# Performance work log

Measured on AMD Instinct MI355X. Metric: run time of the kernel, lower is better.

The kernel has to match this reference:

```python
import jax, jax.numpy as jnp
import numpy as np

B, T, F, H, O = 64, 2048, 128, 512, 4
G = 4 * H  # gates: i, f, g, o (PyTorch order)


def setup_inputs() -> dict:
    key = jax.random.key(0)
    ks = jax.random.split(key, 12)
    s = 1.0 / np.sqrt(H)  # PyTorch LSTM init scale
    return {
        "x": jax.random.normal(ks[0], (B, T, F), dtype=jnp.float32),
        "W_ih_l0": jax.random.uniform(ks[1], (G, F), jnp.float32, -s, s),
        "W_hh_l0": jax.random.uniform(ks[2], (G, H), jnp.float32, -s, s),
        "b_ih_l0": jax.random.uniform(ks[3], (G,), jnp.float32, -s, s),
        "b_hh_l0": jax.random.uniform(ks[4], (G,), jnp.float32, -s, s),
        "W_ih_l1": jax.random.uniform(ks[5], (G, H), jnp.float32, -s, s),
        "W_hh_l1": jax.random.uniform(ks[6], (G, H), jnp.float32, -s, s),
        "b_ih_l1": jax.random.uniform(ks[7], (G,), jnp.float32, -s, s),
        "b_hh_l1": jax.random.uniform(ks[8], (G,), jnp.float32, -s, s),
        "W_out": jax.random.uniform(ks[9], (O, H), jnp.float32, -s, s),
        "b_out": jax.random.uniform(ks[10], (O,), jnp.float32, -s, s),
    }


def lstm_layer(x_seq, W_ih, W_hh, b_ih, b_hh):
    # x_seq: [B, T, Fin] -> (h_seq [B, T, H], h_final [B, H])
    b = x_seq.shape[0]
    h_dim = W_hh.shape[1]
    # Precompute input projections for all timesteps in one big GEMM.
    x_proj = jnp.einsum('btf,gf->btg', x_seq, W_ih) + b_ih + b_hh  # [B, T, 4H]

    def step(carry, xp_t):
        h, c = carry
        gates = xp_t + h @ W_hh.T  # [B, 4H]
        i, f, g, o = jnp.split(gates, 4, axis=-1)
        i = jax.nn.sigmoid(i)
        f = jax.nn.sigmoid(f)
        g = jnp.tanh(g)
        o = jax.nn.sigmoid(o)
        c = f * c + i * g
        h = o * jnp.tanh(c)
        return (h, c), h

    h0 = jnp.zeros((b, h_dim), x_seq.dtype)
    c0 = jnp.zeros((b, h_dim), x_seq.dtype)
    (hT, _), hs = jax.lax.scan(step, (h0, c0), jnp.swapaxes(x_proj, 0, 1))
    return jnp.swapaxes(hs, 0, 1), hT


def reference(x, W_ih_l0, W_hh_l0, b_ih_l0, b_hh_l0,
              W_ih_l1, W_hh_l1, b_ih_l1, b_hh_l1, W_out, b_out):
    h0_seq, h0_final = lstm_layer(x, W_ih_l0, W_hh_l0, b_ih_l0, b_hh_l0)
    _, h1_final = lstm_layer(h0_seq, W_ih_l1, W_hh_l1, b_ih_l1, b_hh_l1)
    # hn = stack([h0_final, h1_final]); relu(hn); linear applied to hn[0]
    hn0 = jax.nn.relu(h0_final)  # [B, H]
    out = hn0 @ W_out.T + b_out  # [B, 4]
    return out
```

## Files before the change

### kernel.cpp

```cpp
#include <hip/hip_runtime.h>
#include <hip/hip_bf16.h>
#include <cstdint>
#include <cstddef>


#define B_ 64
#define T_ 2048
#define F_ 128
#define H_ 512

#define NBLK 128
#define NTHR 256

#define ACT_STRIDE 1280
#define SMEM_SZ (16 * ACT_STRIDE)
#define HSLOT (B_ * H_)

typedef __bf16 bf16;
typedef __bf16 bf16x4 __attribute__((ext_vector_type(4)));
typedef __bf16 bf16x8 __attribute__((ext_vector_type(8)));
typedef float f32x4 __attribute__((ext_vector_type(4)));
typedef unsigned int u32;
typedef u32 u32x2 __attribute__((ext_vector_type(2)));
typedef u32 u32x4 __attribute__((ext_vector_type(4)));

static __device__ __forceinline__ float sigm(float v) {
  return 1.f / (1.f + __expf(-v));
}
static __device__ __forceinline__ float tanh_f(float v) {
  float a = fminf(fabsf(v), 20.f);
  float e = __expf(-2.f * a);
  float t = 1.f - 2.f * e / (1.f + e);
  return copysignf(t, v);
}
static __device__ __forceinline__ u32 bf16bits(float f) {
  bf16 b = (bf16)f;
  unsigned short us;
  __builtin_memcpy(&us, &b, 2);
  return (u32)us;
}

__global__ void __launch_bounds__(NTHR) prep_kernel(u32* hbuf) {
  int idx = blockIdx.x * blockDim.x + threadIdx.x;
  hbuf[idx] = 0u;
}

__global__ void __launch_bounds__(NTHR) xconv_kernel(
    const float* __restrict__ x, bf16* __restrict__ xbf) {
  const int b = blockIdx.x;
  const int t0 = blockIdx.y * 256;
  const int f2 = threadIdx.x & 63;
  const int tq = threadIdx.x >> 6;
  const int rg = b >> 4, row = b & 15;
  for (int i = 0; i < 64; ++i) {
    int t = t0 + i * 4 + tq;
    float2 xv = *(const float2*)(x + ((size_t)b * T_ + t) * F_ + 2 * f2);
    u32 w = bf16bits(xv.x) | (bf16bits(xv.y) << 16);
    *(u32*)((char*)xbf + ((((size_t)t * 4 + rg) * 16 + row) * 128 + 2 * f2) * 2) = w;
  }
}

__global__ void __launch_bounds__(NTHR, 1) lstm_kernel(
    const float* __restrict__ x,
    const float* __restrict__ Wih,
    const float* __restrict__ Whh,
    const float* __restrict__ bih,
    const float* __restrict__ bhh,
    u32* __restrict__ hbuf,
    float* __restrict__ hf32,
    const bf16* __restrict__ xbf)
{
  __shared__ __align__(16) char smem[SMEM_SZ];

  const int tid = threadIdx.x;
  const int bid = blockIdx.x;
  const int rg = bid >> 5;
  const int jg = bid & 31;
  const int row0 = rg * 16;
  const int j0 = jg * 16;

  const int lane = tid & 63;
  const int wave = tid >> 6;
  const int fr = lane & 15;
  const int kg = lane >> 4;

  bf16x8 wfrag[20];
  {
    const int G = (fr >> 2) * H_ + j0 + wave * 4 + (fr & 3);
    const float* sih = Wih + (size_t)G * F_;
    const float* shh = Whh + (size_t)G * H_;
    #pragma unroll
    for (int kk = 0; kk < 20; ++kk) {
      const float* s = (kk < 4) ? (sih + kk * 32 + kg * 8)
                                : (shh + (kk - 4) * 32 + kg * 8);
      float4 f0 = *(const float4*)s;
      float4 f1 = *(const float4*)(s + 4);
      bf16x8 w = { (bf16)f0.x, (bf16)f0.y, (bf16)f0.z, (bf16)f0.w,
                   (bf16)f1.x, (bf16)f1.y, (bf16)f1.z, (bf16)f1.w };
      wfrag[kk] = w;
    }
  }

  const int jcol = j0 + wave * 4 + kg;
  const float bi_ = bih[0 * H_ + jcol] + bhh[0 * H_ + jcol];
  const float bf_ = bih[1 * H_ + jcol] + bhh[1 * H_ + jcol];
  const float bg_ = bih[2 * H_ + jcol] + bhh[2 * H_ + jcol];
  const float bo_ = bih[3 * H_ + jcol] + bhh[3 * H_ + jcol];

  const int prow = tid >> 4;
  const int pw = tid & 15;
  const int r0x = tid >> 5;
  const int c40 = tid & 31;
  const float* xp0 = x + (size_t)(row0 + r0x) * T_ * F_ + c40 * 4;
  const float* xp1 = x + (size_t)(row0 + r0x + 8) * T_ * F_ + c40 * 4;
  const int xw0 = r0x * ACT_STRIDE + ((8 * c40) ^ ((r0x & 7) << 4));
  const int xw1 = (r0x + 8) * ACT_STRIDE + ((8 * c40) ^ (((r0x + 8) & 7) << 4));
  const int xrow = tid >> 4;
  const int xseg = tid & 15;
  const int xw = xrow * ACT_STRIDE + ((xseg * 16) ^ ((xrow & 7) << 4));

  char* buf = smem;
  float c_state = 0.f;

  for (int t = 0; t < T_; ++t) {
    if (xbf) {
      u32x4 xv = *(const u32x4*)((const char*)xbf
                  + ((size_t)t * 4 + rg) * 4096 + tid * 16);
      *(u32x4*)(buf + xw) = xv;
    } else {
      float4 xv0 = *(const float4*)(xp0 + (size_t)t * F_);
      float4 xv1 = *(const float4*)(xp1 + (size_t)t * F_);
      bf16x4 b0 = { (bf16)xv0.x, (bf16)xv0.y, (bf16)xv0.z, (bf16)xv0.w };
      bf16x4 b1 = { (bf16)xv1.x, (bf16)xv1.y, (bf16)xv1.z, (bf16)xv1.w };
      *(bf16x4*)(buf + xw0) = b0;
      *(bf16x4*)(buf + xw1) = b1;
    }
    __syncthreads();

    u32x4 v0, v1, v2, v3, v4, v5, v6, v7;
    const u32* hb = hbuf + (size_t)(t & 1) * HSLOT + (size_t)(row0 + prow) * H_ + 4 * pw;
    #define ISSUE_POLLS()                                                               \
      asm volatile("global_load_dwordx4 %0, %1, off sc0 sc1" : "=v"(v0) : "v"(hb));      \
      asm volatile("global_load_dwordx4 %0, %1, off offset:256 sc0 sc1" : "=v"(v1) : "v"(hb)); \
      asm volatile("global_load_dwordx4 %0, %1, off offset:512 sc0 sc1" : "=v"(v2) : "v"(hb)); \
      asm volatile("global_load_dwordx4 %0, %1, off offset:768 sc0 sc1" : "=v"(v3) : "v"(hb)); \
      asm volatile("global_load_dwordx4 %0, %1, off offset:1024 sc0 sc1" : "=v"(v4) : "v"(hb)); \
      asm volatile("global_load_dwordx4 %0, %1, off offset:1280 sc0 sc1" : "=v"(v5) : "v"(hb)); \
      asm volatile("global_load_dwordx4 %0, %1, off offset:1536 sc0 sc1" : "=v"(v6) : "v"(hb)); \
      asm volatile("global_load_dwordx4 %0, %1, off offset:1792 sc0 sc1" : "=v"(v7) : "v"(hb))
    ISSUE_POLLS();
    __builtin_amdgcn_sched_barrier(0);

    f32x4 a0 = {0.f, 0.f, 0.f, 0.f}, a1 = {0.f, 0.f, 0.f, 0.f};
    const char* bbase = buf + fr * ACT_STRIDE;
    const int bmask = (fr & 7) << 4;
    {
      bf16x8 p0 = *(const bf16x8*)(bbase + ((0 * 64 + kg * 16) ^ bmask));
      a0 = __builtin_amdgcn_mfma_f32_16x16x32_bf16(wfrag[0], p0, a0, 0, 0, 0);
      bf16x8 p1 = *(const bf16x8*)(bbase + ((1 * 64 + kg * 16) ^ bmask));
      a1 = __builtin_amdgcn_mfma_f32_16x16x32_bf16(wfrag[1], p1, a1, 0, 0, 0);
      bf16x8 p2 = *(const bf16x8*)(bbase + ((2 * 64 + kg * 16) ^ bmask));
      a0 = __builtin_amdgcn_mfma_f32_16x16x32_bf16(wfrag[2], p2, a0, 0, 0, 0);
      bf16x8 p3 = *(const bf16x8*)(bbase + ((3 * 64 + kg * 16) ^ bmask));
      a1 = __builtin_amdgcn_mfma_f32_16x16x32_bf16(wfrag[3], p3, a1, 0, 0, 0);
    }
    __builtin_amdgcn_sched_barrier(0);

    {
      const u32 tgt = (u32)t << 16;
      for (;;) {
        asm volatile("s_waitcnt vmcnt(0)" ::: "memory");
        __builtin_amdgcn_sched_barrier(0);
        u32 m0 = v0[0]; m0 = m0 < v0[1] ? m0 : v0[1];
        u32 m1 = v0[2]; m1 = m1 < v0[3] ? m1 : v0[3];
        #define MIN4(V) { m0 = m0 < V[0] ? m0 : V[0]; m0 = m0 < V[1] ? m0 : V[1]; \
                          m1 = m1 < V[2] ? m1 : V[2]; m1 = m1 < V[3] ? m1 : V[3]; }
        MIN4(v1) MIN4(v2) MIN4(v3) MIN4(v4) MIN4(v5) MIN4(v6) MIN4(v7)
        #undef MIN4
        u32 m = m0 < m1 ? m0 : m1;
        if (m >= tgt) break;
        ISSUE_POLLS();
      }
    }
    #undef ISSUE_POLLS

    {
      char* dst = buf + prow * ACT_STRIDE;
      const int swz = (prow & 7) << 4;
      #define UNPACK(i, V)                                                  \
        {                                                                   \
          u32 w0 = (V[0] & 0xffffu) | (V[1] << 16);                         \
          u32 w1 = (V[2] & 0xffffu) | (V[3] << 16);                         \
          u32x2 wp = { w0, w1 };                                            \
          *(u32x2*)(dst + ((256 + 128 * (i) + 8 * pw) ^ swz)) = wp;         \
        }
      UNPACK(0, v0) UNPACK(1, v1) UNPACK(2, v2) UNPACK(3, v3)
      UNPACK(4, v4) UNPACK(5, v5) UNPACK(6, v6) UNPACK(7, v7)
      #undef UNPACK
    }
    __syncthreads();

    #pragma unroll
    for (int kk = 4; kk < 20; kk += 2) {
      bf16x8 b0 = *(const bf16x8*)(bbase + ((kk * 64 + kg * 16) ^ bmask));
      a0 = __builtin_amdgcn_mfma_f32_16x16x32_bf16(wfrag[kk], b0, a0, 0, 0, 0);
      bf16x8 b1 = *(const bf16x8*)(bbase + (((kk + 1) * 64 + kg * 16) ^ bmask));
      a1 = __builtin_amdgcn_mfma_f32_16x16x32_bf16(wfrag[kk + 1], b1, a1, 0, 0, 0);
    }
    f32x4 dsum = a0 + a1;

    float d0 = dsum[0], d1 = dsum[1], d2 = dsum[2], d3 = dsum[3];
    float t0 = __shfl_xor((kg & 2) ? d0 : d2, 32, 64);
    float t1 = __shfl_xor((kg & 2) ? d1 : d3, 32, 64);
    float w0 = (kg & 2) ? t0 : d0;
    float w1 = (kg & 2) ? t1 : d1;
    float w2 = (kg & 2) ? d2 : t0;
    float w3 = (kg & 2) ? d3 : t1;
    float t2 = __shfl_xor((kg & 1) ? w0 : w1, 16, 64);
    float t3 = __shfl_xor((kg & 1) ? w2 : w3, 16, 64);
    float gi = (kg & 1) ? t2 : w0;
    float gf = (kg & 1) ? w1 : t2;
    float gg = (kg & 1) ? t3 : w2;
    float go = (kg & 1) ? w3 : t3;

    float iv = sigm(gi + bi_);
    float fv = sigm(gf + bf_);
    float gv = tanh_f(gg + bg_);
    float ov = sigm(go + bo_);
    c_state = fv * c_state + iv * gv;
    float hv = ov * tanh_f(c_state);

    u32 val = ((u32)(t + 1) << 16) | bf16bits(hv);
    u32* dstp = hbuf + (size_t)((t + 1) & 1) * HSLOT + (size_t)(row0 + fr) * H_ + jcol;
    asm volatile("global_store_dword %0, %1, off sc0 sc1" :: "v"(dstp), "v"(val) : "memory");

    if (t == T_ - 1) hf32[(size_t)(row0 + fr) * H_ + jcol] = hv;
  }
}

__global__ void __launch_bounds__(64) out_kernel(
    const float* __restrict__ h_f32,
    const float* __restrict__ Wout,
    const float* __restrict__ bout,
    float* __restrict__ out)
{
  int b = blockIdx.x;
  int lane = threadIdx.x;
  float a0 = 0.f, a1 = 0.f, a2 = 0.f, a3 = 0.f;
  for (int j = lane; j < H_; j += 64) {
    float hv = fmaxf(h_f32[(size_t)b * H_ + j], 0.f);
    a0 += hv * Wout[0 * H_ + j];
    a1 += hv * Wout[1 * H_ + j];
    a2 += hv * Wout[2 * H_ + j];
    a3 += hv * Wout[3 * H_ + j];
  }
  #pragma unroll
  for (int off = 32; off; off >>= 1) {
    a0 += __shfl_down(a0, off);
    a1 += __shfl_down(a1, off);
    a2 += __shfl_down(a2, off);
    a3 += __shfl_down(a3, off);
  }
  if (lane == 0) {
    out[b * 4 + 0] = a0 + bout[0];
    out[b * 4 + 1] = a1 + bout[1];
    out[b * 4 + 2] = a2 + bout[2];
    out[b * 4 + 3] = a3 + bout[3];
  }
}

extern "C" void kernel_launch(void* const* d_in, const int* in_sizes, int n_in,
                              void* d_out, int out_size, void* d_ws, size_t ws_size,
                              hipStream_t stream) {
  const float* x    = (const float*)d_in[0];
  const float* Wih  = (const float*)d_in[1];
  const float* Whh  = (const float*)d_in[2];
  const float* bih  = (const float*)d_in[3];
  const float* bhh  = (const float*)d_in[4];
  const float* Wout = (const float*)d_in[9];
  const float* bout = (const float*)d_in[10];

  char* ws = (char*)d_ws;
  u32*   hbuf = (u32*)ws;
  float* hf32 = (float*)(ws + 262144);
  const size_t XBF_OFF = 393216;
  const size_t XBF_SZ = (size_t)T_ * 4 * 16 * 128 * 2;
  bf16* xbf = (ws_size >= XBF_OFF + XBF_SZ) ? (bf16*)(ws + XBF_OFF) : nullptr;

  hipLaunchKernelGGL(prep_kernel, dim3(256), dim3(NTHR), 0, stream, hbuf);
  if (xbf)
    hipLaunchKernelGGL(xconv_kernel, dim3(64, 8), dim3(NTHR), 0, stream, x, xbf);

  void* args[] = { (void*)&x, (void*)&Wih, (void*)&Whh, (void*)&bih, (void*)&bhh,
                   (void*)&hbuf, (void*)&hf32, (void*)&xbf };
  hipLaunchCooperativeKernel((void*)lstm_kernel, dim3(NBLK), dim3(NTHR),
                             args, 0, stream);

  hipLaunchKernelGGL(out_kernel, dim3(B_), dim3(64), 0, stream,
                     hf32, Wout, bout, (float*)d_out);
}
```

Measured before the change: 4.204 ms.

## Replace tagged-hidden-state polling with per-step arrival counters and packed bf16 h

The old scheme embedded a step tag in each 32-bit h word, so every wave polled and min-reduced 8 dwordx4 loads per iteration. Now h is stored as plain bf16 and each wave increments a per-row-group counter after its store. Consumers spin on a single counter dword, then fetch half as many h bytes and write them straight to LDS without unpacking. This adds an extra waitcnt plus an atomic per wave per step, serialises the h fetch behind the counter, and includes a guard break that could silently proceed on timeout.

Result: slower. 7.285 ms (+73.3%).

```diff
diff --git a/kernel.cpp b/kernel.cpp
--- a/kernel.cpp
+++ b/kernel.cpp
@@ -14,14 +14,12 @@
 
 #define ACT_STRIDE 1280
 #define SMEM_SZ (16 * ACT_STRIDE)
-#define HSLOT (B_ * H_)
 
 typedef __bf16 bf16;
 typedef __bf16 bf16x4 __attribute__((ext_vector_type(4)));
 typedef __bf16 bf16x8 __attribute__((ext_vector_type(8)));
 typedef float f32x4 __attribute__((ext_vector_type(4)));
 typedef unsigned int u32;
-typedef u32 u32x2 __attribute__((ext_vector_type(2)));
 typedef u32 u32x4 __attribute__((ext_vector_type(4)));
 
 static __device__ __forceinline__ float sigm(float v) {
@@ -40,9 +38,10 @@
   return (u32)us;
 }
 
-__global__ void __launch_bounds__(NTHR) prep_kernel(u32* hbuf) {
+__global__ void __launch_bounds__(NTHR) prep_kernel(u32* hbuf_words, u32* cnt) {
   int idx = blockIdx.x * blockDim.x + threadIdx.x;
-  hbuf[idx] = 0u;
+  hbuf_words[idx] = 0u;
+  if (idx < 16384) cnt[idx] = ((idx & 4095) == 0) ? 128u : 0u;
 }
 
 __global__ void __launch_bounds__(NTHR) xconv_kernel(
@@ -66,7 +65,8 @@
     const float* __restrict__ Whh,
     const float* __restrict__ bih,
     const float* __restrict__ bhh,
-    u32* __restrict__ hbuf,
+    bf16* __restrict__ hbuf,
+    u32* __restrict__ cnt,
     float* __restrict__ hf32,
     const bf16* __restrict__ xbf)
 {
@@ -115,99 +115,90 @@
   const float* xp1 = x + (size_t)(row0 + r0x + 8) * T_ * F_ + c40 * 4;
   const int xw0 = r0x * ACT_STRIDE + ((8 * c40) ^ ((r0x & 7) << 4));
   const int xw1 = (r0x + 8) * ACT_STRIDE + ((8 * c40) ^ (((r0x + 8) & 7) << 4));
-  const int xrow = tid >> 4;
-  const int xseg = tid & 15;
-  const int xw = xrow * ACT_STRIDE + ((xseg * 16) ^ ((xrow & 7) << 4));
-
-  char* buf = smem;
+  const int xw = prow * ACT_STRIDE + ((pw * 16) ^ ((prow & 7) << 4));
+
+  const char* bbase = smem + fr * ACT_STRIDE;
+  const int bmask = (fr & 7) << 4;
+  u32* cgrp = cnt + (rg << 12);
+
   float c_state = 0.f;
 
   for (int t = 0; t < T_; ++t) {
     if (xbf) {
       u32x4 xv = *(const u32x4*)((const char*)xbf
                   + ((size_t)t * 4 + rg) * 4096 + tid * 16);
-      *(u32x4*)(buf + xw) = xv;
+      *(u32x4*)(smem + xw) = xv;
     } else {
       float4 xv0 = *(const float4*)(xp0 + (size_t)t * F_);
       float4 xv1 = *(const float4*)(xp1 + (size_t)t * F_);
       bf16x4 b0 = { (bf16)xv0.x, (bf16)xv0.y, (bf16)xv0.z, (bf16)xv0.w };
       bf16x4 b1 = { (bf16)xv1.x, (bf16)xv1.y, (bf16)xv1.z, (bf16)xv1.w };
-      *(bf16x4*)(buf + xw0) = b0;
-      *(bf16x4*)(buf + xw1) = b1;
+      *(bf16x4*)(smem + xw0) = b0;
+      *(bf16x4*)(smem + xw1) = b1;
     }
     __syncthreads();
 
-    u32x4 v0, v1, v2, v3, v4, v5, v6, v7;
-    const u32* hb = hbuf + (size_t)(t & 1) * HSLOT + (size_t)(row0 + prow) * H_ + 4 * pw;
-    #define ISSUE_POLLS()                                                               \
-      asm volatile("global_load_dwordx4 %0, %1, off sc0 sc1" : "=v"(v0) : "v"(hb));      \
-      asm volatile("global_load_dwordx4 %0, %1, off offset:256 sc0 sc1" : "=v"(v1) : "v"(hb)); \
-      asm volatile("global_load_dwordx4 %0, %1, off offset:512 sc0 sc1" : "=v"(v2) : "v"(hb)); \
-      asm volatile("global_load_dwordx4 %0, %1, off offset:768 sc0 sc1" : "=v"(v3) : "v"(hb)); \
-      asm volatile("global_load_dwordx4 %0, %1, off offset:1024 sc0 sc1" : "=v"(v4) : "v"(hb)); \
-      asm volatile("global_load_dwordx4 %0, %1, off offset:1280 sc0 sc1" : "=v"(v5) : "v"(hb)); \
-      asm volatile("global_load_dwordx4 %0, %1, off offset:1536 sc0 sc1" : "=v"(v6) : "v"(hb)); \
-      asm volatile("global_load_dwordx4 %0, %1, off offset:1792 sc0 sc1" : "=v"(v7) : "v"(hb))
-    ISSUE_POLLS();
-    __builtin_amdgcn_sched_barrier(0);
+    u32 cv;
+    const u32* cp = cgrp + t;
+    asm volatile("global_load_dword %0, %1, off sc0 sc1" : "=v"(cv) : "v"(cp));
 
     f32x4 a0 = {0.f, 0.f, 0.f, 0.f}, a1 = {0.f, 0.f, 0.f, 0.f};
-    const char* bbase = buf + fr * ACT_STRIDE;
-    const int bmask = (fr & 7) << 4;
+    f32x4 a2 = {0.f, 0.f, 0.f, 0.f}, a3 = {0.f, 0.f, 0.f, 0.f};
     {
       bf16x8 p0 = *(const bf16x8*)(bbase + ((0 * 64 + kg * 16) ^ bmask));
       a0 = __builtin_amdgcn_mfma_f32_16x16x32_bf16(wfrag[0], p0, a0, 0, 0, 0);
       bf16x8 p1 = *(const bf16x8*)(bbase + ((1 * 64 + kg * 16) ^ bmask));
       a1 = __builtin_amdgcn_mfma_f32_16x16x32_bf16(wfrag[1], p1, a1, 0, 0, 0);
-      bf16x8 p2 = *(const bf16x8*)(bbase + ((2 * 64 + kg * 16) ^ bmask));
-      a0 = __builtin_amdgcn_mfma_f32_16x16x32_bf16(wfrag[2], p2, a0, 0, 0, 0);
-      bf16x8 p3 = *(const bf16x8*)(bbase + ((3 * 64 + kg * 16) ^ bmask));
-      a1 = __builtin_amdgcn_mfma_f32_16x16x32_bf16(wfrag[3], p3, a1, 0, 0, 0);
-    }
-    __builtin_amdgcn_sched_barrier(0);
-
-    {
-      const u32 tgt = (u32)t << 16;
+    }
+    {
+      int guard = 0;
       for (;;) {
         asm volatile("s_waitcnt vmcnt(0)" ::: "memory");
         __builtin_amdgcn_sched_barrier(0);
-        u32 m0 = v0[0]; m0 = m0 < v0[1] ? m0 : v0[1];
-        u32 m1 = v0[2]; m1 = m1 < v0[3] ? m1 : v0[3];
-        #define MIN4(V) { m0 = m0 < V[0] ? m0 : V[0]; m0 = m0 < V[1] ? m0 : V[1]; \
-                          m1 = m1 < V[2] ? m1 : V[2]; m1 = m1 < V[3] ? m1 : V[3]; }
-        MIN4(v1) MIN4(v2) MIN4(v3) MIN4(v4) MIN4(v5) MIN4(v6) MIN4(v7)
-        #undef MIN4
-        u32 m = m0 < m1 ? m0 : m1;
-        if (m >= tgt) break;
-        ISSUE_POLLS();
+        if (cv >= 128u) break;
+        if (++guard > (1 << 22)) break;
+        asm volatile("global_load_dword %0, %1, off sc0 sc1" : "=v"(cv) : "v"(cp));
       }
     }
-    #undef ISSUE_POLLS
-
-    {
-      char* dst = buf + prow * ACT_STRIDE;
+
+    u32x4 v0, v1, v2, v3;
+    const char* hb = (const char*)hbuf + ((size_t)(t & 1) << 16)
+                   + (size_t)(row0 + prow) * 1024 + pw * 16;
+    asm volatile("global_load_dwordx4 %0, %1, off sc0 sc1"             : "=v"(v0) : "v"(hb));
+    asm volatile("global_load_dwordx4 %0, %1, off offset:256 sc0 sc1"  : "=v"(v1) : "v"(hb));
+    asm volatile("global_load_dwordx4 %0, %1, off offset:512 sc0 sc1"  : "=v"(v2) : "v"(hb));
+    asm volatile("global_load_dwordx4 %0, %1, off offset:768 sc0 sc1"  : "=v"(v3) : "v"(hb));
+    {
+      bf16x8 p2 = *(const bf16x8*)(bbase + ((2 * 64 + kg * 16) ^ bmask));
+      a2 = __builtin_amdgcn_mfma_f32_16x16x32_bf16(wfrag[2], p2, a2, 0, 0, 0);
+      bf16x8 p3 = *(const bf16x8*)(bbase + ((3 * 64 + kg * 16) ^ bmask));
+      a3 = __builtin_amdgcn_mfma_f32_16x16x32_bf16(wfrag[3], p3, a3, 0, 0, 0);
+    }
+    asm volatile("s_waitcnt vmcnt(0)" ::: "memory");
+    __builtin_amdgcn_sched_barrier(0);
+
+    {
+      char* dst = smem + prow * ACT_STRIDE;
       const int swz = (prow & 7) << 4;
-      #define UNPACK(i, V)                                                  \
-        {                                                                   \
-          u32 w0 = (V[0] & 0xffffu) | (V[1] << 16);                         \
-          u32 w1 = (V[2] & 0xffffu) | (V[3] << 16);                         \
-          u32x2 wp = { w0, w1 };                                            \
-          *(u32x2*)(dst + ((256 + 128 * (i) + 8 * pw) ^ swz)) = wp;         \
-        }
-      UNPACK(0, v0) UNPACK(1, v1) UNPACK(2, v2) UNPACK(3, v3)
-      UNPACK(4, v4) UNPACK(5, v5) UNPACK(6, v6) UNPACK(7, v7)
-      #undef UNPACK
+      *(u32x4*)(dst + ((256 + 0 * 256 + 16 * pw) ^ swz)) = v0;
+      *(u32x4*)(dst + ((256 + 1 * 256 + 16 * pw) ^ swz)) = v1;
+      *(u32x4*)(dst + ((256 + 2 * 256 + 16 * pw) ^ swz)) = v2;
+      *(u32x4*)(dst + ((256 + 3 * 256 + 16 * pw) ^ swz)) = v3;
     }
     __syncthreads();
 
     #pragma unroll
-    for (int kk = 4; kk < 20; kk += 2) {
-      bf16x8 b0 = *(const bf16x8*)(bbase + ((kk * 64 + kg * 16) ^ bmask));
-      a0 = __builtin_amdgcn_mfma_f32_16x16x32_bf16(wfrag[kk], b0, a0, 0, 0, 0);
+    for (int kk = 4; kk < 20; kk += 4) {
+      bf16x8 b0 = *(const bf16x8*)(bbase + (((kk + 0) * 64 + kg * 16) ^ bmask));
+      a0 = __builtin_amdgcn_mfma_f32_16x16x32_bf16(wfrag[kk + 0], b0, a0, 0, 0, 0);
       bf16x8 b1 = *(const bf16x8*)(bbase + (((kk + 1) * 64 + kg * 16) ^ bmask));
       a1 = __builtin_amdgcn_mfma_f32_16x16x32_bf16(wfrag[kk + 1], b1, a1, 0, 0, 0);
-    }
-    f32x4 dsum = a0 + a1;
+      bf16x8 b2 = *(const bf16x8*)(bbase + (((kk + 2) * 64 + kg * 16) ^ bmask));
+      a2 = __builtin_amdgcn_mfma_f32_16x16x32_bf16(wfrag[kk + 2], b2, a2, 0, 0, 0);
+      bf16x8 b3 = *(const bf16x8*)(bbase + (((kk + 3) * 64 + kg * 16) ^ bmask));
+      a3 = __builtin_amdgcn_mfma_f32_16x16x32_bf16(wfrag[kk + 3], b3, a3, 0, 0, 0);
+    }
+    f32x4 dsum = (a0 + a1) + (a2 + a3);
 
     float d0 = dsum[0], d1 = dsum[1], d2 = dsum[2], d3 = dsum[3];
     float t0 = __shfl_xor((kg & 2) ? d0 : d2, 32, 64);
@@ -230,11 +221,17 @@
     c_state = fv * c_state + iv * gv;
     float hv = ov * tanh_f(c_state);
 
-    u32 val = ((u32)(t + 1) << 16) | bf16bits(hv);
-    u32* dstp = hbuf + (size_t)((t + 1) & 1) * HSLOT + (size_t)(row0 + fr) * H_ + jcol;
-    asm volatile("global_store_dword %0, %1, off sc0 sc1" :: "v"(dstp), "v"(val) : "memory");
-
+    {
+      u32 hbits = bf16bits(hv);
+      char* dstp = (char*)hbuf + ((size_t)((t + 1) & 1) << 16)
+                 + (size_t)(row0 + fr) * 1024 + jcol * 2;
+      asm volatile("global_store_short %0, %1, off sc0 sc1"
+                   :: "v"(dstp), "v"(hbits) : "memory");
+    }
     if (t == T_ - 1) hf32[(size_t)(row0 + fr) * H_ + jcol] = hv;
+    asm volatile("s_waitcnt vmcnt(0)" ::: "memory");
+    __builtin_amdgcn_sched_barrier(0);
+    if (lane == 0) atomicAdd(cgrp + t + 1, 1u);
   }
 }
 
@@ -281,18 +278,20 @@
   const float* bout = (const float*)d_in[10];
 
   char* ws = (char*)d_ws;
-  u32*   hbuf = (u32*)ws;
-  float* hf32 = (float*)(ws + 262144);
+  bf16*  hbuf = (bf16*)ws;
+  float* hf32 = (float*)(ws + 131072);
+  u32*   cnt  = (u32*)(ws + 262144);
   const size_t XBF_OFF = 393216;
   const size_t XBF_SZ = (size_t)T_ * 4 * 16 * 128 * 2;
   bf16* xbf = (ws_size >= XBF_OFF + XBF_SZ) ? (bf16*)(ws + XBF_OFF) : nullptr;
 
-  hipLaunchKernelGGL(prep_kernel, dim3(256), dim3(NTHR), 0, stream, hbuf);
+  hipLaunchKernelGGL(prep_kernel, dim3(NBLK), dim3(NTHR), 0, stream,
+                     (u32*)hbuf, cnt);
   if (xbf)
     hipLaunchKernelGGL(xconv_kernel, dim3(64, 8), dim3(NTHR), 0, stream, x, xbf);
 
   void* args[] = { (void*)&x, (void*)&Wih, (void*)&Whh, (void*)&bih, (void*)&bhh,
-                   (void*)&hbuf, (void*)&hf32, (void*)&xbf };
+                   (void*)&hbuf, (void*)&cnt, (void*)&hf32, (void*)&xbf };
   hipLaunchCooperativeKernel((void*)lstm_kernel, dim3(NBLK), dim3(NTHR),
                              args, 0, stream);
 
```

## Repartition LSTM recurrence onto 32 larger blocks with two column tiles per wave

Applied to the files above, without the earlier changes.

Recurrent kernel now runs on 32 blocks of 512 threads instead of 128 blocks of 256. Each wave computes two 4-column hidden tiles, reuses each activation fragment across two MFMAs and spreads accumulation over four chains. The goal is fewer participants in the cross-block flag polling and less redundant h-state reading per step, at the cost of more per-block work and register pressure. A bounded-iteration guard is added to the spin-wait loop.

Result: slower. 7.959 ms (+89.3%).

```diff
diff --git a/kernel.cpp b/kernel.cpp
--- a/kernel.cpp
+++ b/kernel.cpp
@@ -9,8 +9,10 @@
 #define F_ 128
 #define H_ 512
 
-#define NBLK 128
-#define NTHR 256
+#define NBLK 32
+#define NTHR 512
+#define ROWS 16
+#define JU 64
 
 #define ACT_STRIDE 1280
 #define SMEM_SZ (16 * ACT_STRIDE)
@@ -45,7 +47,7 @@
   hbuf[idx] = 0u;
 }
 
-__global__ void __launch_bounds__(NTHR) xconv_kernel(
+__global__ void __launch_bounds__(256) xconv_kernel(
     const float* __restrict__ x, bf16* __restrict__ xbf) {
   const int b = blockIdx.x;
   const int t0 = blockIdx.y * 256;
@@ -74,19 +76,20 @@
 
   const int tid = threadIdx.x;
   const int bid = blockIdx.x;
-  const int rg = bid >> 5;
-  const int jg = bid & 31;
-  const int row0 = rg * 16;
-  const int j0 = jg * 16;
+  const int rg = bid >> 3;
+  const int jg = bid & 7;
+  const int row0 = rg * ROWS;
+  const int j0 = jg * JU;
 
   const int lane = tid & 63;
   const int wave = tid >> 6;
   const int fr = lane & 15;
   const int kg = lane >> 4;
 
-  bf16x8 wfrag[20];
-  {
-    const int G = (fr >> 2) * H_ + j0 + wave * 4 + (fr & 3);
+  bf16x8 wfrag0[20], wfrag1[20];
+  #pragma unroll
+  for (int tau = 0; tau < 2; ++tau) {
+    const int G = (fr >> 2) * H_ + j0 + 8 * wave + 4 * tau + (fr & 3);
     const float* sih = Wih + (size_t)G * F_;
     const float* shh = Whh + (size_t)G * H_;
     #pragma unroll
@@ -97,145 +100,183 @@
       float4 f1 = *(const float4*)(s + 4);
       bf16x8 w = { (bf16)f0.x, (bf16)f0.y, (bf16)f0.z, (bf16)f0.w,
                    (bf16)f1.x, (bf16)f1.y, (bf16)f1.z, (bf16)f1.w };
-      wfrag[kk] = w;
-    }
-  }
-
-  const int jcol = j0 + wave * 4 + kg;
-  const float bi_ = bih[0 * H_ + jcol] + bhh[0 * H_ + jcol];
-  const float bf_ = bih[1 * H_ + jcol] + bhh[1 * H_ + jcol];
-  const float bg_ = bih[2 * H_ + jcol] + bhh[2 * H_ + jcol];
-  const float bo_ = bih[3 * H_ + jcol] + bhh[3 * H_ + jcol];
-
-  const int prow = tid >> 4;
-  const int pw = tid & 15;
-  const int r0x = tid >> 5;
-  const int c40 = tid & 31;
-  const float* xp0 = x + (size_t)(row0 + r0x) * T_ * F_ + c40 * 4;
-  const float* xp1 = x + (size_t)(row0 + r0x + 8) * T_ * F_ + c40 * 4;
-  const int xw0 = r0x * ACT_STRIDE + ((8 * c40) ^ ((r0x & 7) << 4));
-  const int xw1 = (r0x + 8) * ACT_STRIDE + ((8 * c40) ^ (((r0x + 8) & 7) << 4));
-  const int xrow = tid >> 4;
-  const int xseg = tid & 15;
-  const int xw = xrow * ACT_STRIDE + ((xseg * 16) ^ ((xrow & 7) << 4));
-
-  char* buf = smem;
-  float c_state = 0.f;
+      if (tau == 0) wfrag0[kk] = w; else wfrag1[kk] = w;
+    }
+  }
+
+  const int jc0 = j0 + 8 * wave + kg;
+  const int jc1 = jc0 + 4;
+  const float bi0 = bih[0 * H_ + jc0] + bhh[0 * H_ + jc0];
+  const float bf0 = bih[1 * H_ + jc0] + bhh[1 * H_ + jc0];
+  const float bg0 = bih[2 * H_ + jc0] + bhh[2 * H_ + jc0];
+  const float bo0 = bih[3 * H_ + jc0] + bhh[3 * H_ + jc0];
+  const float bi1 = bih[0 * H_ + jc1] + bhh[0 * H_ + jc1];
+  const float bf1 = bih[1 * H_ + jc1] + bhh[1 * H_ + jc1];
+  const float bg1 = bih[2 * H_ + jc1] + bhh[2 * H_ + jc1];
+  const float bo1 = bih[3 * H_ + jc1] + bhh[3 * H_ + jc1];
+
+  const int prow = tid >> 5;
+  const int pw = tid & 31;
+  const int swz = (prow & 7) << 4;
+  const float* xfall = x + (size_t)(row0 + prow) * T_ * F_ + pw * 4;
+  const int xwf = prow * ACT_STRIDE + ((8 * pw) ^ swz);
+
+  const char* bbase = smem + fr * ACT_STRIDE;
+  const int bmask = (fr & 7) << 4;
+
+  float c0 = 0.f, c1 = 0.f;
+
+#define ISSUE_POLLS() do { \
+    asm volatile("global_load_dwordx4 %0, %1, off sc0 sc1"            : "=v"(v0) : "v"(hb)); \
+    asm volatile("global_load_dwordx4 %0, %1, off offset:16 sc0 sc1"  : "=v"(v1) : "v"(hb)); \
+    asm volatile("global_load_dwordx4 %0, %1, off offset:32 sc0 sc1"  : "=v"(v2) : "v"(hb)); \
+    asm volatile("global_load_dwordx4 %0, %1, off offset:48 sc0 sc1"  : "=v"(v3) : "v"(hb)); \
+  } while (0)
 
   for (int t = 0; t < T_; ++t) {
     if (xbf) {
-      u32x4 xv = *(const u32x4*)((const char*)xbf
-                  + ((size_t)t * 4 + rg) * 4096 + tid * 16);
-      *(u32x4*)(buf + xw) = xv;
+      u32x2 xv = *(const u32x2*)((const char*)xbf
+                  + ((size_t)t * 4 + rg) * 4096 + tid * 8);
+      *(u32x2*)(smem + xwf) = xv;
     } else {
-      float4 xv0 = *(const float4*)(xp0 + (size_t)t * F_);
-      float4 xv1 = *(const float4*)(xp1 + (size_t)t * F_);
-      bf16x4 b0 = { (bf16)xv0.x, (bf16)xv0.y, (bf16)xv0.z, (bf16)xv0.w };
-      bf16x4 b1 = { (bf16)xv1.x, (bf16)xv1.y, (bf16)xv1.z, (bf16)xv1.w };
-      *(bf16x4*)(buf + xw0) = b0;
-      *(bf16x4*)(buf + xw1) = b1;
+      float4 xv = *(const float4*)(xfall + (size_t)t * F_);
+      bf16x4 bv = { (bf16)xv.x, (bf16)xv.y, (bf16)xv.z, (bf16)xv.w };
+      *(bf16x4*)(smem + xwf) = bv;
     }
     __syncthreads();
 
-    u32x4 v0, v1, v2, v3, v4, v5, v6, v7;
-    const u32* hb = hbuf + (size_t)(t & 1) * HSLOT + (size_t)(row0 + prow) * H_ + 4 * pw;
-    #define ISSUE_POLLS()                                                               \
-      asm volatile("global_load_dwordx4 %0, %1, off sc0 sc1" : "=v"(v0) : "v"(hb));      \
-      asm volatile("global_load_dwordx4 %0, %1, off offset:256 sc0 sc1" : "=v"(v1) : "v"(hb)); \
-      asm volatile("global_load_dwordx4 %0, %1, off offset:512 sc0 sc1" : "=v"(v2) : "v"(hb)); \
-      asm volatile("global_load_dwordx4 %0, %1, off offset:768 sc0 sc1" : "=v"(v3) : "v"(hb)); \
-      asm volatile("global_load_dwordx4 %0, %1, off offset:1024 sc0 sc1" : "=v"(v4) : "v"(hb)); \
-      asm volatile("global_load_dwordx4 %0, %1, off offset:1280 sc0 sc1" : "=v"(v5) : "v"(hb)); \
-      asm volatile("global_load_dwordx4 %0, %1, off offset:1536 sc0 sc1" : "=v"(v6) : "v"(hb)); \
-      asm volatile("global_load_dwordx4 %0, %1, off offset:1792 sc0 sc1" : "=v"(v7) : "v"(hb))
+    u32x4 v0, v1, v2, v3;
+    const u32* hb = hbuf + (size_t)(t & 1) * HSLOT
+                  + (size_t)(row0 + prow) * H_ + 16 * pw;
     ISSUE_POLLS();
     __builtin_amdgcn_sched_barrier(0);
 
-    f32x4 a0 = {0.f, 0.f, 0.f, 0.f}, a1 = {0.f, 0.f, 0.f, 0.f};
-    const char* bbase = buf + fr * ACT_STRIDE;
-    const int bmask = (fr & 7) << 4;
+    f32x4 a00 = {0.f,0.f,0.f,0.f}, a01 = {0.f,0.f,0.f,0.f};
+    f32x4 a02 = {0.f,0.f,0.f,0.f}, a03 = {0.f,0.f,0.f,0.f};
+    f32x4 a10 = {0.f,0.f,0.f,0.f}, a11 = {0.f,0.f,0.f,0.f};
+    f32x4 a12 = {0.f,0.f,0.f,0.f}, a13 = {0.f,0.f,0.f,0.f};
     {
       bf16x8 p0 = *(const bf16x8*)(bbase + ((0 * 64 + kg * 16) ^ bmask));
-      a0 = __builtin_amdgcn_mfma_f32_16x16x32_bf16(wfrag[0], p0, a0, 0, 0, 0);
+      a00 = __builtin_amdgcn_mfma_f32_16x16x32_bf16(wfrag0[0], p0, a00, 0, 0, 0);
+      a10 = __builtin_amdgcn_mfma_f32_16x16x32_bf16(wfrag1[0], p0, a10, 0, 0, 0);
       bf16x8 p1 = *(const bf16x8*)(bbase + ((1 * 64 + kg * 16) ^ bmask));
-      a1 = __builtin_amdgcn_mfma_f32_16x16x32_bf16(wfrag[1], p1, a1, 0, 0, 0);
+      a01 = __builtin_amdgcn_mfma_f32_16x16x32_bf16(wfrag0[1], p1, a01, 0, 0, 0);
+      a11 = __builtin_amdgcn_mfma_f32_16x16x32_bf16(wfrag1[1], p1, a11, 0, 0, 0);
       bf16x8 p2 = *(const bf16x8*)(bbase + ((2 * 64 + kg * 16) ^ bmask));
-      a0 = __builtin_amdgcn_mfma_f32_16x16x32_bf16(wfrag[2], p2, a0, 0, 0, 0);
+      a02 = __builtin_amdgcn_mfma_f32_16x16x32_bf16(wfrag0[2], p2, a02, 0, 0, 0);
+      a12 = __builtin_amdgcn_mfma_f32_16x16x32_bf16(wfrag1[2], p2, a12, 0, 0, 0);
       bf16x8 p3 = *(const bf16x8*)(bbase + ((3 * 64 + kg * 16) ^ bmask));
-      a1 = __builtin_amdgcn_mfma_f32_16x16x32_bf16(wfrag[3], p3, a1, 0, 0, 0);
+      a03 = __builtin_amdgcn_mfma_f32_16x16x32_bf16(wfrag0[3], p3, a03, 0, 0, 0);
+      a13 = __builtin_amdgcn_mfma_f32_16x16x32_bf16(wfrag1[3], p3, a13, 0, 0, 0);
     }
     __builtin_amdgcn_sched_barrier(0);
 
     {
       const u32 tgt = (u32)t << 16;
+      int guard = 0;
       for (;;) {
         asm volatile("s_waitcnt vmcnt(0)" ::: "memory");
         __builtin_amdgcn_sched_barrier(0);
-        u32 m0 = v0[0]; m0 = m0 < v0[1] ? m0 : v0[1];
-        u32 m1 = v0[2]; m1 = m1 < v0[3] ? m1 : v0[3];
+        u32 m0 = v0[0] < v0[1] ? v0[0] : v0[1];
+        u32 m1 = v0[2] < v0[3] ? v0[2] : v0[3];
         #define MIN4(V) { m0 = m0 < V[0] ? m0 : V[0]; m0 = m0 < V[1] ? m0 : V[1]; \
                           m1 = m1 < V[2] ? m1 : V[2]; m1 = m1 < V[3] ? m1 : V[3]; }
-        MIN4(v1) MIN4(v2) MIN4(v3) MIN4(v4) MIN4(v5) MIN4(v6) MIN4(v7)
+        MIN4(v1) MIN4(v2) MIN4(v3)
         #undef MIN4
         u32 m = m0 < m1 ? m0 : m1;
         if (m >= tgt) break;
+        if (++guard > (1 << 22)) break;
         ISSUE_POLLS();
       }
     }
-    #undef ISSUE_POLLS
-
-    {
-      char* dst = buf + prow * ACT_STRIDE;
-      const int swz = (prow & 7) << 4;
-      #define UNPACK(i, V)                                                  \
-        {                                                                   \
-          u32 w0 = (V[0] & 0xffffu) | (V[1] << 16);                         \
-          u32 w1 = (V[2] & 0xffffu) | (V[3] << 16);                         \
-          u32x2 wp = { w0, w1 };                                            \
-          *(u32x2*)(dst + ((256 + 128 * (i) + 8 * pw) ^ swz)) = wp;         \
-        }
-      UNPACK(0, v0) UNPACK(1, v1) UNPACK(2, v2) UNPACK(3, v3)
-      UNPACK(4, v4) UNPACK(5, v5) UNPACK(6, v6) UNPACK(7, v7)
-      #undef UNPACK
+
+    {
+      char* dst = smem + prow * ACT_STRIDE;
+      u32x4 w0 = { (v0[0] & 0xffffu) | (v0[1] << 16),
+                   (v0[2] & 0xffffu) | (v0[3] << 16),
+                   (v1[0] & 0xffffu) | (v1[1] << 16),
+                   (v1[2] & 0xffffu) | (v1[3] << 16) };
+      u32x4 w1 = { (v2[0] & 0xffffu) | (v2[1] << 16),
+                   (v2[2] & 0xffffu) | (v2[3] << 16),
+                   (v3[0] & 0xffffu) | (v3[1] << 16),
+                   (v3[2] & 0xffffu) | (v3[3] << 16) };
+      *(u32x4*)(dst + ((256 + 32 * pw + 0) ^ swz)) = w0;
+      *(u32x4*)(dst + ((256 + 32 * pw + 16) ^ swz)) = w1;
     }
     __syncthreads();
 
     #pragma unroll
-    for (int kk = 4; kk < 20; kk += 2) {
-      bf16x8 b0 = *(const bf16x8*)(bbase + ((kk * 64 + kg * 16) ^ bmask));
-      a0 = __builtin_amdgcn_mfma_f32_16x16x32_bf16(wfrag[kk], b0, a0, 0, 0, 0);
+    for (int kk = 4; kk < 20; kk += 4) {
+      bf16x8 b0 = *(const bf16x8*)(bbase + (((kk + 0) * 64 + kg * 16) ^ bmask));
+      a00 = __builtin_amdgcn_mfma_f32_16x16x32_bf16(wfrag0[kk + 0], b0, a00, 0, 0, 0);
+      a10 = __builtin_amdgcn_mfma_f32_16x16x32_bf16(wfrag1[kk + 0], b0, a10, 0, 0, 0);
       bf16x8 b1 = *(const bf16x8*)(bbase + (((kk + 1) * 64 + kg * 16) ^ bmask));
-      a1 = __builtin_amdgcn_mfma_f32_16x16x32_bf16(wfrag[kk + 1], b1, a1, 0, 0, 0);
-    }
-    f32x4 dsum = a0 + a1;
-
-    float d0 = dsum[0], d1 = dsum[1], d2 = dsum[2], d3 = dsum[3];
-    float t0 = __shfl_xor((kg & 2) ? d0 : d2, 32, 64);
-    float t1 = __shfl_xor((kg & 2) ? d1 : d3, 32, 64);
-    float w0 = (kg & 2) ? t0 : d0;
-    float w1 = (kg & 2) ? t1 : d1;
-    float w2 = (kg & 2) ? d2 : t0;
-    float w3 = (kg & 2) ? d3 : t1;
-    float t2 = __shfl_xor((kg & 1) ? w0 : w1, 16, 64);
-    float t3 = __shfl_xor((kg & 1) ? w2 : w3, 16, 64);
-    float gi = (kg & 1) ? t2 : w0;
-    float gf = (kg & 1) ? w1 : t2;
-    float gg = (kg & 1) ? t3 : w2;
-    float go = (kg & 1) ? w3 : t3;
-
-    float iv = sigm(gi + bi_);
-    float fv = sigm(gf + bf_);
-    float gv = tanh_f(gg + bg_);
-    float ov = sigm(go + bo_);
-    c_state = fv * c_state + iv * gv;
-    float hv = ov * tanh_f(c_state);
-
-    u32 val = ((u32)(t + 1) << 16) | bf16bits(hv);
-    u32* dstp = hbuf + (size_t)((t + 1) & 1) * HSLOT + (size_t)(row0 + fr) * H_ + jcol;
-    asm volatile("global_store_dword %0, %1, off sc0 sc1" :: "v"(dstp), "v"(val) : "memory");
-
-    if (t == T_ - 1) hf32[(size_t)(row0 + fr) * H_ + jcol] = hv;
-  }
+      a01 = __builtin_amdgcn_mfma_f32_16x16x32_bf16(wfrag0[kk + 1], b1, a01, 0, 0, 0);
+      a11 = __builtin_amdgcn_mfma_f32_16x16x32_bf16(wfrag1[kk + 1], b1, a11, 0, 0, 0);
+      bf16x8 b2 = *(const bf16x8*)(bbase + (((kk + 2) * 64 + kg * 16) ^ bmask));
+      a02 = __builtin_amdgcn_mfma_f32_16x16x32_bf16(wfrag0[kk + 2], b2, a02, 0, 0, 0);
+      a12 = __builtin_amdgcn_mfma_f32_16x16x32_bf16(wfrag1[kk + 2], b2, a12, 0, 0, 0);
+      bf16x8 b3 = *(const bf16x8*)(bbase + (((kk + 3) * 64 + kg * 16) ^ bmask));
+      a03 = __builtin_amdgcn_mfma_f32_16x16x32_bf16(wfrag0[kk + 3], b3, a03, 0, 0, 0);
+      a13 = __builtin_amdgcn_mfma_f32_16x16x32_bf16(wfrag1[kk + 3], b3, a13, 0, 0, 0);
+    }
+    f32x4 ds0 = (a00 + a01) + (a02 + a03);
+    f32x4 ds1 = (a10 + a11) + (a12 + a13);
+
+    u32* slot_out = hbuf + (size_t)((t + 1) & 1) * HSLOT + (size_t)(row0 + fr) * H_;
+
+    {
+      float d0 = ds0[0], d1 = ds0[1], d2 = ds0[2], d3 = ds0[3];
+      float t0 = __shfl_xor((kg & 2) ? d0 : d2, 32, 64);
+      float t1 = __shfl_xor((kg & 2) ? d1 : d3, 32, 64);
+      float w0 = (kg & 2) ? t0 : d0;
+      float w1 = (kg & 2) ? t1 : d1;
+      float w2 = (kg & 2) ? d2 : t0;
+      float w3 = (kg & 2) ? d3 : t1;
+      float t2 = __shfl_xor((kg & 1) ? w0 : w1, 16, 64);
+      float t3 = __shfl_xor((kg & 1) ? w2 : w3, 16, 64);
+      float gi = (kg & 1) ? t2 : w0;
+      float gf = (kg & 1) ? w1 : t2;
+      float gg = (kg & 1) ? t3 : w2;
+      float go = (kg & 1) ? w3 : t3;
+      float iv = sigm(gi + bi0);
+      float fv = sigm(gf + bf0);
+      float gv = tanh_f(gg + bg0);
+      float ov = sigm(go + bo0);
+      c0 = fv * c0 + iv * gv;
+      float hv = ov * tanh_f(c0);
+      u32 val = ((u32)(t + 1) << 16) | bf16bits(hv);
+      u32* dstp = slot_out + jc0;
+      asm volatile("global_store_dword %0, %1, off sc0 sc1" :: "v"(dstp), "v"(val) : "memory");
+      if (t == T_ - 1) hf32[(size_t)(row0 + fr) * H_ + jc0] = hv;
+    }
+    {
+      float d0 = ds1[0], d1 = ds1[1], d2 = ds1[2], d3 = ds1[3];
+      float t0 = __shfl_xor((kg & 2) ? d0 : d2, 32, 64);
+      float t1 = __shfl_xor((kg & 2) ? d1 : d3, 32, 64);
+      float w0 = (kg & 2) ? t0 : d0;
+      float w1 = (kg & 2) ? t1 : d1;
+      float w2 = (kg & 2) ? d2 : t0;
+      float w3 = (kg & 2) ? d3 : t1;
+      float t2 = __shfl_xor((kg & 1) ? w0 : w1, 16, 64);
+      float t3 = __shfl_xor((kg & 1) ? w2 : w3, 16, 64);
+      float gi = (kg & 1) ? t2 : w0;
+      float gf = (kg & 1) ? w1 : t2;
+      float gg = (kg & 1) ? t3 : w2;
+      float go = (kg & 1) ? w3 : t3;
+      float iv = sigm(gi + bi1);
+      float fv = sigm(gf + bf1);
+      float gv = tanh_f(gg + bg1);
+      float ov = sigm(go + bo1);
+      c1 = fv * c1 + iv * gv;
+      float hv = ov * tanh_f(c1);
+      u32 val = ((u32)(t + 1) << 16) | bf16bits(hv);
+      u32* dstp = slot_out + jc1;
+      asm volatile("global_store_dword %0, %1, off sc0 sc1" :: "v"(dstp), "v"(val) : "memory");
+      if (t == T_ - 1) hf32[(size_t)(row0 + fr) * H_ + jc1] = hv;
+    }
+  }
+#undef ISSUE_POLLS
 }
 
 __global__ void __launch_bounds__(64) out_kernel(
@@ -287,9 +328,9 @@
   const size_t XBF_SZ = (size_t)T_ * 4 * 16 * 128 * 2;
   bf16* xbf = (ws_size >= XBF_OFF + XBF_SZ) ? (bf16*)(ws + XBF_OFF) : nullptr;
 
-  hipLaunchKernelGGL(prep_kernel, dim3(256), dim3(NTHR), 0, stream, hbuf);
+  hipLaunchKernelGGL(prep_kernel, dim3(128), dim3(NTHR), 0, stream, hbuf);
   if (xbf)
-    hipLaunchKernelGGL(xconv_kernel, dim3(64, 8), dim3(NTHR), 0, stream, x, xbf);
+    hipLaunchKernelGGL(xconv_kernel, dim3(64, 8), dim3(256), 0, stream, x, xbf);
 
   void* args[] = { (void*)&x, (void*)&Wih, (void*)&Whh, (void*)&bih, (void*)&bhh,
                    (void*)&hbuf, (void*)&hf32, (void*)&xbf };
```
